# Kernel tuning notes

Measured on AMD Instinct MI355X. Metric: run time of the kernel, lower is better.

## Reference

```python
import jax, jax.numpy as jnp
import numpy as np

C = 512
CQK = C // 8
B, H, W = 4, 128, 128

def setup_inputs() -> dict:
    key = jax.random.key(0)
    ks = jax.random.split(key, 8)
    x = jax.random.normal(ks[0], (B, C, H, W), dtype=jnp.float32)
    # 1x1 conv weights stored as [out, in]
    Wq = jax.random.normal(ks[1], (CQK, C), dtype=jnp.float32) * (1.0 / np.sqrt(C))
    bq = jax.random.normal(ks[2], (CQK,), dtype=jnp.float32) * 0.01
    Wk = jax.random.normal(ks[3], (CQK, C), dtype=jnp.float32) * (1.0 / np.sqrt(C))
    bk = jax.random.normal(ks[4], (CQK,), dtype=jnp.float32) * 0.01
    Wv = jax.random.normal(ks[5], (C, C), dtype=jnp.float32) * (1.0 / np.sqrt(C))
    bv = jax.random.normal(ks[6], (C,), dtype=jnp.float32) * 0.01
    gamma = jnp.zeros((1,), dtype=jnp.float32)
    return {"x": x, "Wq": Wq, "bq": bq, "Wk": Wk, "bk": bk, "Wv": Wv, "bv": bv, "gamma": gamma}

def _conv1x1(x, Wt, b):
    # x: [B,C,H,W], Wt: [O,C] -> [B,O,H,W]
    return jnp.einsum('bchw,oc->bohw', x, Wt) + b[None, :, None, None]

def reference(x, Wq, bq, Wk, bk, Wv, bv, gamma):
    q = _conv1x1(x, Wq, bq)   # [B,CQK,H,W]
    k = _conv1x1(x, Wk, bk)   # [B,CQK,H,W]
    v = _conv1x1(x, Wv, bv)   # [B,C,H,W]
    # axial attention along height, independently per (batch, width-column)
    energy = jnp.einsum('bchw,bcgw->bwhg', q, k)      # [B,W,H,H]
    attn = jax.nn.softmax(energy, axis=-1)
    out = jnp.einsum('bcgw,bwhg->bchw', v, attn)      # [B,C,H,W]
    return gamma * out + x
```

## Files before the change

kernel.cpp:

```cpp
#include <hip/hip_runtime.h>
#include <hip/hip_bf16.h>

typedef float f32x4  __attribute__((ext_vector_type(4)));
typedef short s16x8  __attribute__((ext_vector_type(8)));
typedef unsigned short u16;

#define B_ 4
#define C_ 512
#define H_ 128
#define W_ 128
#define NO_ 640

__device__ __forceinline__ u16 f2bf(float f) {
    __hip_bfloat16 h = __float2bfloat16(f);
    union { __hip_bfloat16 h; u16 u; } cv; cv.h = h; return cv.u;
}
__device__ __forceinline__ float bf2f(u16 u) {
    union { unsigned u; float f; } cv; cv.u = ((unsigned)u) << 16; return cv.f;
}

__device__ __forceinline__ void gld16(const u16* g, u16* l) {
    __builtin_amdgcn_global_load_lds(
        (const __attribute__((address_space(1))) void*)g,
        (__attribute__((address_space(3))) void*)l, 16, 0, 0);
}

__global__ __launch_bounds__(256) void k_convw(const float* __restrict__ Wq, const float* __restrict__ bq,
                                               const float* __restrict__ Wk, const float* __restrict__ bk,
                                               const float* __restrict__ Wv, const float* __restrict__ bv,
                                               u16* __restrict__ Wcat, float* __restrict__ bcat) {
    const int idx = blockIdx.x * 256 + threadIdx.x;
    if (idx < NO_ * C_) {
        const int o = idx >> 9, c = idx & 511;
        float v;
        if (o < 64)       v = Wq[o * C_ + c];
        else if (o < 128) v = Wk[(o - 64) * C_ + c];
        else              v = Wv[(o - 128) * C_ + c];
        Wcat[idx] = f2bf(v);
    }
    if (idx < NO_) {
        float v = (idx < 64) ? bq[idx] : ((idx < 128) ? bk[idx - 64] : bv[idx - 128]);
        bcat[idx] = v;
    }
}

__global__ __launch_bounds__(256) void k_transpose_x(const float* __restrict__ x, u16* __restrict__ xT) {
    __shared__ float tile[64][65];
    const int b  = blockIdx.x >> 7;
    const int h  = blockIdx.x & 127;
    const int c0 = (blockIdx.y >> 1) * 64;
    const int w0 = (blockIdx.y & 1) * 64;
    const int t = threadIdx.x, r = t >> 4, seg = t & 15;
    const float* xp = x + (size_t)b * C_ * H_ * W_ + (size_t)h * W_;
#pragma unroll
    for (int rr = 0; rr < 4; ++rr) {
        const int c = rr * 16 + r;
        float4 v = *(const float4*)(xp + (size_t)(c0 + c) * (H_ * W_) + w0 + seg * 4);
        tile[c][seg * 4 + 0] = v.x; tile[c][seg * 4 + 1] = v.y;
        tile[c][seg * 4 + 2] = v.z; tile[c][seg * 4 + 3] = v.w;
    }
    __syncthreads();
#pragma unroll
    for (int rr = 0; rr < 4; ++rr) {
        const int w = rr * 16 + r;
        ushort4 u;
        u.x = f2bf(tile[seg * 4 + 0][w]); u.y = f2bf(tile[seg * 4 + 1][w]);
        u.z = f2bf(tile[seg * 4 + 2][w]); u.w = f2bf(tile[seg * 4 + 3][w]);
        *(ushort4*)(xT + ((size_t)((b * W_ + w0 + w) * H_ + h)) * C_ + c0 + seg * 4) = u;
    }
}

__global__ __launch_bounds__(256, 4) void k_gemm(const u16* __restrict__ A, const u16* __restrict__ Wc,
                                                 const float* __restrict__ bias, u16* __restrict__ Call,
                                                 u16* __restrict__ vt) {
    __shared__ __align__(16) u16 smem[17408];
    const int t = threadIdx.x;
    const int lane = t & 63;
    const int wave = t >> 6;
    const int wr = wave >> 1;
    const int wc = wave & 1;
    const int lr = lane & 15;
    const int q4 = lane >> 4;

    const int bid = blockIdx.x;
    const int wg = (bid & 7) * 320 + (bid >> 3);
    const int panel = wg / 5;
    const int n = wg - panel * 5;
    const int r0 = panel * 128;
    const int n0 = n * 128;

    const int srow = t >> 3;
    const int slog = (t & 7) ^ (srow & 7);
    const u16* gA = A  + (size_t)(r0 + srow) * C_ + slog * 8;
    const u16* gB = Wc + (size_t)(n0 + srow) * C_ + slog * 8;

    f32x4 acc[4][4] = {};
#pragma unroll
    for (int T = 0; T < 8; ++T) {
        const int k0 = T * 64;
#pragma unroll
        for (int r = 0; r < 4; ++r) {
            gld16(gA + (size_t)r * 32 * C_ + k0, &smem[r * 2048 + t * 8]);
            gld16(gB + (size_t)r * 32 * C_ + k0, &smem[8192 + r * 2048 + t * 8]);
        }
        __syncthreads();
#pragma unroll
        for (int ksl = 0; ksl < 2; ++ksl) {
            const int sl = ksl * 4 + q4;
            s16x8 fa[4], fb[4];
#pragma unroll
            for (int mi = 0; mi < 4; ++mi) {
                const int rr = wr * 64 + mi * 16 + lr;
                fa[mi] = *(const s16x8*)&smem[rr * 64 + ((sl ^ (rr & 7)) * 8)];
            }
#pragma unroll
            for (int ni = 0; ni < 4; ++ni) {
                const int rr = wc * 64 + ni * 16 + lr;
                fb[ni] = *(const s16x8*)&smem[8192 + rr * 64 + ((sl ^ (rr & 7)) * 8)];
            }
            __builtin_amdgcn_s_setprio(1);
#pragma unroll
            for (int mi = 0; mi < 4; ++mi)
#pragma unroll
                for (int ni = 0; ni < 4; ++ni)
                    acc[mi][ni] = __builtin_amdgcn_mfma_f32_16x16x32_bf16(
                        fa[mi], fb[ni], acc[mi][ni], 0, 0, 0);
            __builtin_amdgcn_s_setprio(0);
        }
        __syncthreads();
    }

    if (n == 0) {
#pragma unroll
        for (int ni = 0; ni < 4; ++ni) {
            const int o = wc * 64 + ni * 16 + lr;
            const float bz = bias[o];
#pragma unroll
            for (int mi = 0; mi < 4; ++mi)
#pragma unroll
                for (int j = 0; j < 4; ++j) {
                    const int rg = r0 + wr * 64 + mi * 16 + q4 * 4 + j;
                    Call[(size_t)rg * 128 + o] = f2bf(acc[mi][ni][j] + bz);
                }
        }
    } else {
        u16* Tt = smem;
#pragma unroll
        for (int ni = 0; ni < 4; ++ni) {
            const int c_loc = wc * 64 + ni * 16 + lr;
            const float bz = bias[n0 + c_loc];
#pragma unroll
            for (int mi = 0; mi < 4; ++mi) {
                const int h = wr * 64 + mi * 16 + q4 * 4;
                ushort4 u4;
                u4.x = f2bf(acc[mi][ni][0] + bz);
                u4.y = f2bf(acc[mi][ni][1] + bz);
                u4.z = f2bf(acc[mi][ni][2] + bz);
                u4.w = f2bf(acc[mi][ni][3] + bz);
                *(ushort4*)&Tt[c_loc * 136 + h] = u4;
            }
        }
        __syncthreads();
        {
            const int c_loc = t >> 1;
            const int half  = t & 1;
            const int cg = (n - 1) * 128 + c_loc;
            u16* dst = vt + ((size_t)panel * 512 + cg) * 128 + half * 64;
            const u16* src = &Tt[c_loc * 136 + half * 64];
#pragma unroll
            for (int k = 0; k < 8; ++k)
                *(s16x8*)&dst[k * 8] = *(const s16x8*)&src[k * 8];
        }
    }
}

__global__ __launch_bounds__(256) void k_attn(const u16* __restrict__ Call, const u16* __restrict__ vt,
                                              u16* __restrict__ outws) {
    __shared__ __align__(16) float E[128][132];
    __shared__ float Rinv[128];
    const int bw = blockIdx.x;
    const int t = threadIdx.x;
    const int lane = t & 63;
    const int wr = t >> 7;
    const int wc = (t >> 6) & 1;
    const int lr = lane & 15, lk = (lane >> 4) * 8;
    const size_t rowbase = (size_t)bw * 128;

    f32x4 e[4][4] = {};
#pragma unroll
    for (int kk = 0; kk < 2; ++kk) {
        s16x8 fq[4], fk[4];
#pragma unroll
        for (int mi = 0; mi < 4; ++mi)
            fq[mi] = *(const s16x8*)&Call[(rowbase + wr * 64 + mi * 16 + lr) * 128 + kk * 32 + lk];
#pragma unroll
        for (int ni = 0; ni < 4; ++ni)
            fk[ni] = *(const s16x8*)&Call[(rowbase + wc * 64 + ni * 16 + lr) * 128 + 64 + kk * 32 + lk];
#pragma unroll
        for (int mi = 0; mi < 4; ++mi)
#pragma unroll
            for (int ni = 0; ni < 4; ++ni)
                e[mi][ni] = __builtin_amdgcn_mfma_f32_16x16x32_bf16(fq[mi], fk[ni], e[mi][ni], 0, 0, 0);
    }
#pragma unroll
    for (int mi = 0; mi < 4; ++mi)
#pragma unroll
        for (int ni = 0; ni < 4; ++ni)
#pragma unroll
            for (int j = 0; j < 4; ++j)
                E[wr * 64 + mi * 16 + (lane >> 4) * 4 + j][wc * 64 + ni * 16 + lr] = e[mi][ni][j];
    __syncthreads();

    {
        const int h = t >> 1, hf = (t & 1) * 64;
        float m = -1e30f;
        for (int i = 0; i < 64; ++i) m = fmaxf(m, E[h][hf + i]);
        m = fmaxf(m, __shfl_xor(m, 1));
        float s = 0.f;
        for (int i = 0; i < 64; ++i) {
            float p = __expf(E[h][hf + i] - m);
            E[h][hf + i] = p;
            s += p;
        }
        s += __shfl_xor(s, 1);
        if ((t & 1) == 0) Rinv[h] = 1.0f / s;
    }
    __syncthreads();

    float rv[4][4];
#pragma unroll
    for (int mi = 0; mi < 4; ++mi)
#pragma unroll
        for (int j = 0; j < 4; ++j)
            rv[mi][j] = Rinv[wr * 64 + mi * 16 + (lane >> 4) * 4 + j];

    s16x8 pa[4][4];
#pragma unroll
    for (int kk = 0; kk < 4; ++kk)
#pragma unroll
        for (int mi = 0; mi < 4; ++mi) {
            const float* ep = &E[wr * 64 + mi * 16 + lr][kk * 32 + lk];
            float4 v0 = *(const float4*)ep;
            float4 v1 = *(const float4*)(ep + 4);
            s16x8 a;
            a[0] = (short)f2bf(v0.x); a[1] = (short)f2bf(v0.y);
            a[2] = (short)f2bf(v0.z); a[3] = (short)f2bf(v0.w);
            a[4] = (short)f2bf(v1.x); a[5] = (short)f2bf(v1.y);
            a[6] = (short)f2bf(v1.z); a[7] = (short)f2bf(v1.w);
            pa[kk][mi] = a;
        }

    for (int cc = 0; cc < 4; ++cc) {
        f32x4 acc[4][4] = {};
#pragma unroll
        for (int kk = 0; kk < 4; ++kk) {
            s16x8 fb[4];
#pragma unroll
            for (int ni = 0; ni < 4; ++ni)
                fb[ni] = *(const s16x8*)&vt[((size_t)bw * 512 + cc * 128 + wc * 64 + ni * 16 + lr) * 128 + kk * 32 + lk];
#pragma unroll
            for (int mi = 0; mi < 4; ++mi)
#pragma unroll
                for (int ni = 0; ni < 4; ++ni)
                    acc[mi][ni] = __builtin_amdgcn_mfma_f32_16x16x32_bf16(pa[kk][mi], fb[ni], acc[mi][ni], 0, 0, 0);
        }
#pragma unroll
        for (int ni = 0; ni < 4; ++ni) {
            const int c = cc * 128 + wc * 64 + ni * 16 + lr;
#pragma unroll
            for (int mi = 0; mi < 4; ++mi)
#pragma unroll
                for (int j = 0; j < 4; ++j) {
                    const int hh = wr * 64 + mi * 16 + (lane >> 4) * 4 + j;
                    outws[(rowbase + hh) * 512 + c] = f2bf(acc[mi][ni][j] * rv[mi][j]);
                }
        }
    }
}

__global__ __launch_bounds__(256) void k_merge(const u16* __restrict__ outws, const float* __restrict__ x,
                                               const float* __restrict__ gamma, float* __restrict__ out) {
    __shared__ float tile[64][65];
    const int b  = blockIdx.x >> 7;
    const int h  = blockIdx.x & 127;
    const int c0 = (blockIdx.y >> 1) * 64;
    const int w0 = (blockIdx.y & 1) * 64;
    const float g = gamma[0];
    const int t = threadIdx.x, r = t >> 4, seg = t & 15;
#pragma unroll
    for (int rr = 0; rr < 4; ++rr) {
        const int w = rr * 16 + r;
        ushort4 v = *(const ushort4*)(outws + ((size_t)((b * W_ + w0 + w) * H_) + h) * C_ + c0 + seg * 4);
        tile[w][seg * 4 + 0] = bf2f(v.x); tile[w][seg * 4 + 1] = bf2f(v.y);
        tile[w][seg * 4 + 2] = bf2f(v.z); tile[w][seg * 4 + 3] = bf2f(v.w);
    }
    __syncthreads();
#pragma unroll
    for (int rr = 0; rr < 4; ++rr) {
        const int c = rr * 16 + r;
        const size_t base = ((size_t)(b * C_ + c0 + c) * H_ + h) * W_ + w0 + seg * 4;
        float4 xv = *(const float4*)(x + base);
        float4 o;
        o.x = g * tile[seg * 4 + 0][c] + xv.x;
        o.y = g * tile[seg * 4 + 1][c] + xv.y;
        o.z = g * tile[seg * 4 + 2][c] + xv.z;
        o.w = g * tile[seg * 4 + 3][c] + xv.w;
        *(float4*)(out + base) = o;
    }
}

extern "C" void kernel_launch(void* const* d_in, const int* in_sizes, int n_in,
                              void* d_out, int out_size, void* d_ws, size_t ws_size,
                              hipStream_t stream) {
    const float* x     = (const float*)d_in[0];
    const float* Wq    = (const float*)d_in[1];
    const float* bq    = (const float*)d_in[2];
    const float* Wk    = (const float*)d_in[3];
    const float* bk    = (const float*)d_in[4];
    const float* Wv    = (const float*)d_in[5];
    const float* bv    = (const float*)d_in[6];
    const float* gamma = (const float*)d_in[7];

    char* ws = (char*)d_ws;
    u16*   Wcat  = (u16*)ws;
    float* bcat  = (float*)(ws + 655360);
    u16*   xT    = (u16*)(ws + (1u << 20));
    u16*   Call  = (u16*)(ws + (1u << 20) + 67108864);
    u16*   outws = xT;
    u16*   vt    = (u16*)d_out;

    k_convw<<<dim3((NO_ * C_ + 255) / 256), 256, 0, stream>>>(Wq, bq, Wk, bk, Wv, bv, Wcat, bcat);
    k_transpose_x<<<dim3(B_ * H_, 16), 256, 0, stream>>>(x, xT);
    k_gemm<<<dim3(2560), 256, 0, stream>>>(xT, Wcat, bcat, Call, vt);
    k_attn<<<dim3(B_ * W_), 256, 0, stream>>>(Call, vt, outws);
    k_merge<<<dim3(B_ * H_, 16), 256, 0, stream>>>(outws, x, gamma, (float*)d_out);
}
```

Baseline: 192.5 us.

## Double-buffer LDS tiles in projection GEMM with K=32 steps

```diff
diff --git a/kernel.cpp b/kernel.cpp
--- a/kernel.cpp
+++ b/kernel.cpp
@@ -89,46 +89,52 @@
     const int r0 = panel * 128;
     const int n0 = n * 128;
 
-    const int srow = t >> 3;
-    const int slog = (t & 7) ^ (srow & 7);
+    const int srow = t >> 2;
+    const int slog = (t & 3) ^ (srow & 3);
     const u16* gA = A  + (size_t)(r0 + srow) * C_ + slog * 8;
     const u16* gB = Wc + (size_t)(n0 + srow) * C_ + slog * 8;
 
+#define STAGE(KT) do {                                               \
+        u16* S_ = smem + ((KT) & 1) * 8192;                          \
+        const int k0_ = (KT) * 32;                                   \
+        gld16(gA + k0_,                   S_ + t * 8);               \
+        gld16(gA + (size_t)64 * C_ + k0_, S_ + 2048 + t * 8);        \
+        gld16(gB + k0_,                   S_ + 4096 + t * 8);        \
+        gld16(gB + (size_t)64 * C_ + k0_, S_ + 6144 + t * 8);        \
+    } while (0)
+
     f32x4 acc[4][4] = {};
-#pragma unroll
-    for (int T = 0; T < 8; ++T) {
-        const int k0 = T * 64;
-#pragma unroll
-        for (int r = 0; r < 4; ++r) {
-            gld16(gA + (size_t)r * 32 * C_ + k0, &smem[r * 2048 + t * 8]);
-            gld16(gB + (size_t)r * 32 * C_ + k0, &smem[8192 + r * 2048 + t * 8]);
-        }
-        __syncthreads();
-#pragma unroll
-        for (int ksl = 0; ksl < 2; ++ksl) {
-            const int sl = ksl * 4 + q4;
-            s16x8 fa[4], fb[4];
-#pragma unroll
-            for (int mi = 0; mi < 4; ++mi) {
-                const int rr = wr * 64 + mi * 16 + lr;
-                fa[mi] = *(const s16x8*)&smem[rr * 64 + ((sl ^ (rr & 7)) * 8)];
-            }
-#pragma unroll
-            for (int ni = 0; ni < 4; ++ni) {
-                const int rr = wc * 64 + ni * 16 + lr;
-                fb[ni] = *(const s16x8*)&smem[8192 + rr * 64 + ((sl ^ (rr & 7)) * 8)];
-            }
-            __builtin_amdgcn_s_setprio(1);
-#pragma unroll
-            for (int mi = 0; mi < 4; ++mi)
-#pragma unroll
-                for (int ni = 0; ni < 4; ++ni)
-                    acc[mi][ni] = __builtin_amdgcn_mfma_f32_16x16x32_bf16(
-                        fa[mi], fb[ni], acc[mi][ni], 0, 0, 0);
-            __builtin_amdgcn_s_setprio(0);
-        }
-        __syncthreads();
-    }
+    STAGE(0);
+
+#pragma unroll
+    for (int T = 0; T < 16; ++T) {
+        asm volatile("s_waitcnt vmcnt(0)" ::: "memory");
+        __builtin_amdgcn_s_barrier();
+        const u16* Ab = smem + (T & 1) * 8192;
+        const u16* Bb = Ab + 4096;
+        s16x8 fa[4], fb[4];
+#pragma unroll
+        for (int mi = 0; mi < 4; ++mi) {
+            const int rr = wr * 64 + mi * 16 + lr;
+            fa[mi] = *(const s16x8*)&Ab[rr * 32 + ((q4 ^ (rr & 3)) * 8)];
+        }
+#pragma unroll
+        for (int ni = 0; ni < 4; ++ni) {
+            const int rr = wc * 64 + ni * 16 + lr;
+            fb[ni] = *(const s16x8*)&Bb[rr * 32 + ((q4 ^ (rr & 3)) * 8)];
+        }
+        if (T < 15) STAGE(T + 1);
+        __builtin_amdgcn_s_setprio(1);
+#pragma unroll
+        for (int mi = 0; mi < 4; ++mi)
+#pragma unroll
+            for (int ni = 0; ni < 4; ++ni)
+                acc[mi][ni] = __builtin_amdgcn_mfma_f32_16x16x32_bf16(
+                    fa[mi], fb[ni], acc[mi][ni], 0, 0, 0);
+        __builtin_amdgcn_s_setprio(0);
+    }
+#undef STAGE
+    __syncthreads();
 
     if (n == 0) {
 #pragma unroll
```

New measurement: 197.7 us. 1.03x slower.
